# Kernel tuning notes

Hardware: AMD Instinct MI355X
Metric: run time of the kernel (lower is better)

Reference implementation:

```python
import jax, jax.numpy as jnp
import numpy as np

B, D = 65536, 1024

def setup_inputs() -> dict:
    key = jax.random.key(0)
    x = jax.random.normal(key, (B, D), dtype=jnp.float32)
    return {"x": x}

def reference(x) -> jnp.ndarray:
    d = x.shape[1]
    # suffix_norm[:, i] = ||x[:, i:]|| via reverse cumulative sum of squares (single O(D) pass)
    suffix_norm = jnp.sqrt(jnp.cumsum((x * x)[:, ::-1], axis=1)[:, ::-1])
    r = suffix_norm[:, :1]                                   # [B, 1] full norm
    phi = jnp.arccos(x[:, : d - 1] / suffix_norm[:, : d - 1])  # [B, D-1]
    # last angle gets sign correction from the final coordinate
    phi_last = jnp.where(x[:, -1] < 0, 2.0 * jnp.pi - phi[:, -1], phi[:, -1])
    return jnp.concatenate([r, phi[:, : d - 2], phi_last[:, None]], axis=1)
```

## Files before the change

### kernel.cpp

```cpp
#include <hip/hip_runtime.h>
#include <math.h>


#define D_DIM 1024
#define TPB 256
#define RPB 4
#define NG 4

typedef float v4f __attribute__((ext_vector_type(4)));

__device__ __forceinline__ float ang(float num, float den) {
    float r = num * rsqrtf(den);
    r = fminf(1.0f, fmaxf(-1.0f, r));
    return acosf(r);
}

__global__ __launch_bounds__(TPB) void tohypersphere_kernel(
    const float* __restrict__ x, float* __restrict__ out, int n_rows) {
    const int lane = threadIdx.x & 63;
    const int wv   = threadIdx.x >> 6;
    const int row  = blockIdx.x * RPB + wv;
    if (row >= n_rows) return;

    const float4* __restrict__ xp = (const float4*)(x + (size_t)row * D_DIM);

    float4 v[NG];
#pragma unroll
    for (int k = 0; k < NG; ++k) v[k] = xp[64 * k + lane];

    float s0[NG], s1[NG], s2[NG], s3[NG];
#pragma unroll
    for (int k = 0; k < NG; ++k) {
        s3[k] = v[k].w * v[k].w;
        s2[k] = fmaf(v[k].z, v[k].z, s3[k]);
        s1[k] = fmaf(v[k].y, v[k].y, s2[k]);
        s0[k] = fmaf(v[k].x, v[k].x, s1[k]);
    }

    float tot[NG];
#pragma unroll
    for (int k = 0; k < NG; ++k) tot[k] = s0[k];
#pragma unroll
    for (int o = 1; o < 64; o <<= 1) {
#pragma unroll
        for (int k = 0; k < NG; ++k) {
            float n = __shfl_down(tot[k], o, 64);
            if (lane + o < 64) tot[k] += n;
        }
    }

    float G[NG];
#pragma unroll
    for (int k = 0; k < NG; ++k) G[k] = __shfl(tot[k], 0, 64);

    float base[NG];
    float after = 0.0f;
#pragma unroll
    for (int k = NG - 1; k >= 0; --k) {
        base[k] = (tot[k] - s0[k]) + after;
        after += G[k];
    }

    float xup[NG], xpg[NG];
#pragma unroll
    for (int k = 0; k < NG; ++k) xup[k] = __shfl_up(v[k].w, 1, 64);
#pragma unroll
    for (int k = 0; k < NG; ++k) xpg[k] = __shfl(v[(k + NG - 1) % NG].w, 63, 64);

    v4f* __restrict__ op = (v4f*)(out + (size_t)row * D_DIM);
#pragma unroll
    for (int k = 0; k < NG; ++k) {
        const float suf0 = s0[k] + base[k];
        float o0, o1, o2, o3;
        if (k == 0 && lane == 0) {
            o0 = sqrtf(suf0);
        } else {
            const float xprev = (lane == 0) ? xpg[k] : xup[k];
            o0 = ang(xprev, fmaf(xprev, xprev, suf0));
        }
        o1 = ang(v[k].x, suf0);
        o2 = ang(v[k].y, s1[k] + base[k]);
        o3 = ang(v[k].z, s2[k] + base[k]);
        if (k == NG - 1 && lane == 63 && v[k].w < 0.0f) {
            o3 = 6.283185307179586476f - o3;
        }
        v4f t = {o0, o1, o2, o3};
        __builtin_nontemporal_store(t, op + 64 * k + lane);
    }
}

extern "C" void kernel_launch(void* const* d_in, const int* in_sizes, int n_in,
                              void* d_out, int out_size, void* d_ws, size_t ws_size,
                              hipStream_t stream) {
    const float* x = (const float*)d_in[0];
    float* out = (float*)d_out;
    const int B = in_sizes[0] / D_DIM;
    const int grid = (B + RPB - 1) / RPB;
    tohypersphere_kernel<<<grid, TPB, 0, stream>>>(x, out, B);
}
```

Baseline: 437.9 us.

## Use DPP suffix scan, readlane broadcasts, polynomial acos, and regular stores

```diff
diff --git a/kernel.cpp b/kernel.cpp
--- a/kernel.cpp
+++ b/kernel.cpp
@@ -9,10 +9,35 @@
 
 typedef float v4f __attribute__((ext_vector_type(4)));
 
+template <int CTRL>
+__device__ __forceinline__ float dpp0(float x) {
+    return __builtin_bit_cast(
+        float, __builtin_amdgcn_update_dpp(0, __builtin_bit_cast(int, x),
+                                           CTRL, 0xF, 0xF, true));
+}
+
+__device__ __forceinline__ float rdlane(float x, int l) {
+    return __builtin_bit_cast(
+        float, __builtin_amdgcn_readlane(__builtin_bit_cast(int, x), l));
+}
+
+__device__ __forceinline__ float fast_acos(float x) {
+    float a = fabsf(x);
+    float p = fmaf(a, -0.0012624911f, 0.0066700901f);
+    p = fmaf(p, a, -0.0170881256f);
+    p = fmaf(p, a, 0.0308918810f);
+    p = fmaf(p, a, -0.0501743046f);
+    p = fmaf(p, a, 0.0889789874f);
+    p = fmaf(p, a, -0.2145988016f);
+    p = fmaf(p, a, 1.5707963050f);
+    float r = sqrtf(1.0f - a) * p;
+    return x < 0.0f ? 3.14159274101257f - r : r;
+}
+
 __device__ __forceinline__ float ang(float num, float den) {
     float r = num * rsqrtf(den);
     r = fminf(1.0f, fmaxf(-1.0f, r));
-    return acosf(r);
+    return fast_acos(r);
 }
 
 __global__ __launch_bounds__(TPB) void tohypersphere_kernel(
@@ -28,44 +53,60 @@
 #pragma unroll
     for (int k = 0; k < NG; ++k) v[k] = xp[64 * k + lane];
 
-    float s0[NG], s1[NG], s2[NG], s3[NG];
+    float s0[NG], s1[NG], s2[NG];
 #pragma unroll
     for (int k = 0; k < NG; ++k) {
-        s3[k] = v[k].w * v[k].w;
-        s2[k] = fmaf(v[k].z, v[k].z, s3[k]);
+        float s3 = v[k].w * v[k].w;
+        s2[k] = fmaf(v[k].z, v[k].z, s3);
         s1[k] = fmaf(v[k].y, v[k].y, s2[k]);
         s0[k] = fmaf(v[k].x, v[k].x, s1[k]);
     }
 
-    float tot[NG];
+    float ts[NG];
 #pragma unroll
-    for (int k = 0; k < NG; ++k) tot[k] = s0[k];
+    for (int k = 0; k < NG; ++k) ts[k] = s0[k];
 #pragma unroll
-    for (int o = 1; o < 64; o <<= 1) {
+    for (int k = 0; k < NG; ++k) ts[k] += dpp0<0x101>(ts[k]);
 #pragma unroll
-        for (int k = 0; k < NG; ++k) {
-            float n = __shfl_down(tot[k], o, 64);
-            if (lane + o < 64) tot[k] += n;
-        }
+    for (int k = 0; k < NG; ++k) ts[k] += dpp0<0x102>(ts[k]);
+#pragma unroll
+    for (int k = 0; k < NG; ++k) ts[k] += dpp0<0x104>(ts[k]);
+#pragma unroll
+    for (int k = 0; k < NG; ++k) ts[k] += dpp0<0x108>(ts[k]);
+
+    float R[NG][4];
+#pragma unroll
+    for (int k = 0; k < NG; ++k) {
+        R[k][0] = rdlane(ts[k], 0);
+        R[k][1] = rdlane(ts[k], 16);
+        R[k][2] = rdlane(ts[k], 32);
+        R[k][3] = rdlane(ts[k], 48);
     }
+    const int r16 = lane >> 4;
 
     float G[NG];
 #pragma unroll
-    for (int k = 0; k < NG; ++k) G[k] = __shfl(tot[k], 0, 64);
+    for (int k = 0; k < NG; ++k) G[k] = (R[k][0] + R[k][1]) + (R[k][2] + R[k][3]);
+    float ag[NG];
+    ag[NG - 1] = 0.0f;
+#pragma unroll
+    for (int k = NG - 2; k >= 0; --k) ag[k] = ag[k + 1] + G[k + 1];
 
     float base[NG];
-    float after = 0.0f;
 #pragma unroll
-    for (int k = NG - 1; k >= 0; --k) {
-        base[k] = (tot[k] - s0[k]) + after;
-        after += G[k];
+    for (int k = 0; k < NG; ++k) {
+        float af = 0.0f;
+        if (r16 < 1) af += R[k][1];
+        if (r16 < 2) af += R[k][2];
+        if (r16 < 3) af += R[k][3];
+        base[k] = (ts[k] - s0[k]) + af + ag[k];
     }
 
     float xup[NG], xpg[NG];
 #pragma unroll
     for (int k = 0; k < NG; ++k) xup[k] = __shfl_up(v[k].w, 1, 64);
 #pragma unroll
-    for (int k = 0; k < NG; ++k) xpg[k] = __shfl(v[(k + NG - 1) % NG].w, 63, 64);
+    for (int k = 0; k < NG; ++k) xpg[k] = rdlane(v[(k + NG - 1) % NG].w, 63);
 
     v4f* __restrict__ op = (v4f*)(out + (size_t)row * D_DIM);
 #pragma unroll
@@ -85,7 +126,7 @@
             o3 = 6.283185307179586476f - o3;
         }
         v4f t = {o0, o1, o2, o3};
-        __builtin_nontemporal_store(t, op + 64 * k + lane);
+        op[64 * k + lane] = t;
     }
 }
 
```

Measured after the change: 425.2 us. -2.9%, faster.
